# Optimization experiments

Hardware: AMD Instinct MI355X
Metric: run time of the kernel (lower is better)

Reference implementation:

```python
import jax, jax.numpy as jnp
import numpy as np

N_NODES = 50000
N_EDGES = 800000
IN_DIM = 128
HEADS1, D1 = 4, 16   # hidden_dim // 4 = 16, concat -> 64
HID = HEADS1 * D1    # 64
OUT_DIM = 40
NEG_SLOPE = 0.2      # PyG GATConv default


def setup_inputs() -> dict:
    key = jax.random.key(0)
    ks = jax.random.split(key, 11)
    x = jax.random.normal(ks[0], (N_NODES, IN_DIM), dtype=jnp.float32)
    edge_index = jax.random.randint(ks[1], (2, N_EDGES), 0, N_NODES)
    s1 = 1.0 / np.sqrt(IN_DIM)
    s2 = 1.0 / np.sqrt(HID)
    return {
        "x": x,
        "edge_index": edge_index,
        "W1": jax.random.normal(ks[2], (IN_DIM, HEADS1 * D1), dtype=jnp.float32) * s1,
        "a_src1": jax.random.normal(ks[3], (HEADS1, D1), dtype=jnp.float32) * s2,
        "a_dst1": jax.random.normal(ks[4], (HEADS1, D1), dtype=jnp.float32) * s2,
        "b1": jnp.zeros((HID,), dtype=jnp.float32),
        "W2": jax.random.normal(ks[5], (HID, OUT_DIM), dtype=jnp.float32) * s2,
        "a_src2": jax.random.normal(ks[6], (1, OUT_DIM), dtype=jnp.float32) * s2,
        "a_dst2": jax.random.normal(ks[7], (1, OUT_DIM), dtype=jnp.float32) * s2,
        "b2": jnp.zeros((OUT_DIM,), dtype=jnp.float32),
    }


def gat_conv(x, src, dst, W, a_src, a_dst, b, heads, d, n_nodes):
    # linear projection, split into heads: [N, H, d]
    h = (x @ W).reshape(n_nodes, heads, d)
    # per-node attention logits: [N, H]
    alpha_src = jnp.einsum("nhd,hd->nh", h, a_src)
    alpha_dst = jnp.einsum("nhd,hd->nh", h, a_dst)
    # edge attention coefficients
    e = jax.nn.leaky_relu(alpha_src[src] + alpha_dst[dst], NEG_SLOPE)  # [E, H]
    # segment softmax over incoming edges of each destination node
    e_max = jax.ops.segment_max(e, dst, num_segments=n_nodes)
    e_max = jnp.where(jnp.isfinite(e_max), e_max, 0.0)
    e_exp = jnp.exp(e - e_max[dst])
    denom = jax.ops.segment_sum(e_exp, dst, num_segments=n_nodes)
    alpha = e_exp / (denom[dst] + 1e-16)  # [E, H]
    # weighted scatter-aggregate of source messages
    out = jax.ops.segment_sum(h[src] * alpha[..., None], dst, num_segments=n_nodes)
    return out.reshape(n_nodes, heads * d) + b


def reference(x, edge_index, W1, a_src1, a_dst1, b1, W2, a_src2, a_dst2, b2):
    n = x.shape[0]
    # PyG GATConv add_self_loops=True
    loop = jnp.arange(n, dtype=edge_index.dtype)
    src = jnp.concatenate([edge_index[0], loop])
    dst = jnp.concatenate([edge_index[1], loop])
    h = jax.nn.relu(gat_conv(x, src, dst, W1, a_src1, a_dst1, b1, HEADS1, D1, n))
    # dropout is identity in eval mode
    h = gat_conv(h, src, dst, W2, a_src2, a_dst2, b2, 1, OUT_DIM, n)
    return jax.nn.log_softmax(h, axis=1)
```

## Files before the change

### kernel.cpp

```cpp
#include <hip/hip_runtime.h>
#include <hip/hip_fp16.h>
#include <math.h>

#define NN    50000
#define NE0   800000
#define NE    850000
#define INDIM 128
#define HID   64
#define OUTD  40

#define NB    391
#define BSH   7
#define BCAP  3072

typedef unsigned short u16;

union __align__(16) SMa {
    struct { float Wl[INDIM * HID]; float xs[64 * 132]; } g;
    struct { int lh[NB]; int lbase[NB]; unsigned ebuf[3328]; } b;
};

__global__ __launch_bounds__(256, 2) void k_binG1(
    const int* __restrict__ ei, int* __restrict__ bcur, unsigned int* __restrict__ epack,
    const float* __restrict__ x, const float* __restrict__ W1,
    const float* __restrict__ a_s, const float* __restrict__ a_d,
    __half* __restrict__ h1h, float* __restrict__ asrc1, float* __restrict__ adst1)
{
    __shared__ SMa sm;
    const int tid = threadIdx.x;

    if (blockIdx.x < 256) {
        const int CH = (NE + 255) / 256;
        const int e0 = blockIdx.x * CH;
        const int e1 = (e0 + CH < NE) ? e0 + CH : NE;
        const int cnt = e1 - e0;

        for (int i = tid; i < NB; i += 256) sm.b.lh[i] = 0;
        __syncthreads();
        for (int i = tid; i < cnt; i += 256) {
            int e = e0 + i;
            int src, dst;
            if (e < NE0) { src = ei[e]; dst = ei[NE0 + e]; }
            else         { src = e - NE0; dst = src; }
            int bkt = dst >> BSH;
            sm.b.ebuf[i] = (unsigned)src | ((unsigned)(dst & 127) << 16) | ((unsigned)bkt << 23);
            atomicAdd(&sm.b.lh[bkt], 1);
        }
        __syncthreads();
        for (int i = tid; i < NB; i += 256) {
            int c = sm.b.lh[i];
            sm.b.lbase[i] = c ? (i * BCAP + atomicAdd(&bcur[i], c)) : 0;
            sm.b.lh[i] = 0;
        }
        __syncthreads();
        for (int i = tid; i < cnt; i += 256) {
            unsigned rec = sm.b.ebuf[i];
            int bkt = rec >> 23;
            int lpos = atomicAdd(&sm.b.lh[bkt], 1);
            epack[sm.b.lbase[bkt] + lpos] = rec & 0x7FFFFFu;
        }
        return;
    }

    const int r0 = (blockIdx.x - 256) * 64;

    const float4* W4 = (const float4*)W1;
    float4* Wl4 = (float4*)sm.g.Wl;
#pragma unroll
    for (int i = 0; i < 8; ++i) Wl4[tid + i * 256] = W4[tid + i * 256];

    const float4* x4 = (const float4*)x;
#pragma unroll
    for (int i = 0; i < 8; ++i) {
        int idx = tid + i * 256;
        int row = idx >> 5;
        int k4  = idx & 31;
        int nr = r0 + row;
        float4 v = make_float4(0.f, 0.f, 0.f, 0.f);
        if (nr < NN) v = x4[(size_t)nr * 32 + k4];
        *(float4*)&sm.g.xs[row * 132 + k4 * 4] = v;
    }
    __syncthreads();

    const int rg = tid >> 4;
    const int cg = tid & 15;
    const int c4 = cg * 4;
    const float as0 = a_s[c4], as1v = a_s[c4+1], as2v = a_s[c4+2], as3v = a_s[c4+3];
    const float ad0 = a_d[c4], ad1v = a_d[c4+1], ad2v = a_d[c4+2], ad3v = a_d[c4+3];

    float acc[4][4];
#pragma unroll
    for (int i = 0; i < 4; ++i)
#pragma unroll
        for (int j = 0; j < 4; ++j) acc[i][j] = 0.f;

#pragma unroll 4
    for (int k4 = 0; k4 < 32; ++k4) {
        float4 xv[4];
#pragma unroll
        for (int i = 0; i < 4; ++i)
            xv[i] = *(const float4*)&sm.g.xs[(rg * 4 + i) * 132 + k4 * 4];
        const float* wp = &sm.g.Wl[(k4 * 4) * HID + c4];
        float4 w0 = *(const float4*)(wp);
        float4 w1 = *(const float4*)(wp + HID);
        float4 w2 = *(const float4*)(wp + 2 * HID);
        float4 w3 = *(const float4*)(wp + 3 * HID);
#pragma unroll
        for (int i = 0; i < 4; ++i) {
            acc[i][0] += xv[i].x * w0.x + xv[i].y * w1.x + xv[i].z * w2.x + xv[i].w * w3.x;
            acc[i][1] += xv[i].x * w0.y + xv[i].y * w1.y + xv[i].z * w2.y + xv[i].w * w3.y;
            acc[i][2] += xv[i].x * w0.z + xv[i].y * w1.z + xv[i].z * w2.z + xv[i].w * w3.z;
            acc[i][3] += xv[i].x * w0.w + xv[i].y * w1.w + xv[i].z * w2.w + xv[i].w * w3.w;
        }
    }

#pragma unroll
    for (int i = 0; i < 4; ++i) {
        const int n = r0 + rg * 4 + i;
        if (n < NN) {
            __half2 ha = __floats2half2_rn(acc[i][0], acc[i][1]);
            __half2 hb = __floats2half2_rn(acc[i][2], acc[i][3]);
            *(__half2*)&h1h[(size_t)n * HID + c4]     = ha;
            *(__half2*)&h1h[(size_t)n * HID + c4 + 2] = hb;
        }
        float ps = acc[i][0] * as0 + acc[i][1] * as1v + acc[i][2] * as2v + acc[i][3] * as3v;
        float pd = acc[i][0] * ad0 + acc[i][1] * ad1v + acc[i][2] * ad2v + acc[i][3] * ad3v;
        ps += __shfl_xor(ps, 1); ps += __shfl_xor(ps, 2);
        pd += __shfl_xor(pd, 1); pd += __shfl_xor(pd, 2);
        if ((cg & 3) == 0 && n < NN) {
            int head = cg >> 2;
            asrc1[n * 4 + head] = ps;
            adst1[n * 4 + head] = pd;
        }
    }
}

__global__ __launch_bounds__(256) void k_csr(
    const int* __restrict__ bcur, const unsigned int* __restrict__ epack,
    int* __restrict__ off_s, int* __restrict__ off_e, u16* __restrict__ esrc)
{
    __shared__ int lh[128];
    __shared__ int lcur[128];
    __shared__ int sblk;
    const int tid = threadIdx.x, lane = tid & 63;
    const int b = blockIdx.x;
    const int e0 = b * BCAP;
    const int cnt = bcur[b];

    if (tid < 128) lh[tid] = 0;
    __syncthreads();
    for (int i = tid; i < cnt; i += 256)
        atomicAdd(&lh[epack[e0 + i] >> 16], 1);
    __syncthreads();

    int v = 0, incl = 0;
    if (tid < 128) {
        v = lh[tid];
        incl = v;
#pragma unroll
        for (int s = 1; s < 64; s <<= 1) {
            int t = __shfl_up(incl, s);
            if (lane >= s) incl += t;
        }
    }
    if (tid == 63) sblk = incl;
    __syncthreads();
    if (tid >= 64 && tid < 128) incl += sblk;
    if (tid < 128) {
        int ex = e0 + incl - v;
        lcur[tid] = ex;
        int gd = b * 128 + tid;
        if (gd < NN) { off_s[gd] = ex; off_e[gd] = ex + v; }
    }
    __syncthreads();

    for (int i = tid; i < cnt; i += 256) {
        unsigned int p = epack[e0 + i];
        int pos = atomicAdd(&lcur[p >> 16], 1);
        esrc[pos] = (u16)(p & 0xFFFFu);
    }
}

__global__ __launch_bounds__(256) void k_fagg1g2(
    const int* __restrict__ off_s, const int* __restrict__ off_e,
    const u16* __restrict__ esrc, const float* __restrict__ asrc1,
    const float* __restrict__ adst1,
    const __half* __restrict__ h1h, const float* __restrict__ b1,
    const float* __restrict__ W2, const float* __restrict__ a_s2,
    const float* __restrict__ a_d2,
    __half* __restrict__ h2h, float* __restrict__ asrc2, float* __restrict__ adst2)
{
    __shared__ __align__(16) float W2l[HID * OUTD];
    __shared__ __align__(16) float hml[16][72];
    __shared__ float s_a2s[OUTD], s_a2d[OUTD];
    __shared__ float s_ps[16], s_pd[16];
    const int tid = threadIdx.x;

    {
        const float4* W24 = (const float4*)W2;
        float4* W2l4 = (float4*)W2l;
        for (int i = tid; i < (HID * OUTD) / 4; i += 256) W2l4[i] = W24[i];
        if (tid < OUTD) { s_a2s[tid] = a_s2[tid]; s_a2d[tid] = a_d2[tid]; }
        if (tid < 16)   { s_ps[tid] = 0.f; s_pd[tid] = 0.f; }
    }

    const int wv = tid >> 6, lane = tid & 63;
    const int g = lane >> 4, li = lane & 15;
    const int r = wv * 4 + g;
    const int n = blockIdx.x * 16 + r;
    const int s0 = off_s[n], s1 = off_e[n];
    const int hp = li >> 2;
    const float adst = adst1[n * 4 + hp];
    const int last = s1 - 1;

    float l = 0.f, a0 = 0.f, a1 = 0.f, a2 = 0.f, a3 = 0.f;
    const char* hb = (const char*)h1h;

    int sxA[8];
#pragma unroll
    for (int j = 0; j < 8; ++j) {
        int ix = s0 + j;
        sxA[j] = esrc[ix < s1 ? ix : last];
    }
    for (int t = s0; t < s1; t += 8) {
        float ax[8];
#pragma unroll
        for (int j = 0; j < 8; ++j) ax[j] = asrc1[sxA[j] * 4 + hp];
        uint2 raw[8];
#pragma unroll
        for (int j = 0; j < 8; ++j)
            raw[j] = *(const uint2*)(hb + ((size_t)sxA[j] * 128 + li * 8));
        int sxB[8];
        const int t2 = t + 8;
#pragma unroll
        for (int j = 0; j < 8; ++j) {
            int ix = t2 + j;
            sxB[j] = esrc[ix < s1 ? ix : last];
        }
#pragma unroll
        for (int j = 0; j < 8; ++j) {
            float e = ax[j] + adst;
            e = (e > 0.f) ? e : 0.2f * e;
            float w = __expf(e);
            w = ((t + j) < s1) ? w : 0.f;
            float2 f0 = __half22float2(*(__half2*)&raw[j].x);
            float2 f1 = __half22float2(*(__half2*)&raw[j].y);
            l  += w;
            a0 += w * f0.x;
            a1 += w * f0.y;
            a2 += w * f1.x;
            a3 += w * f1.y;
        }
#pragma unroll
        for (int j = 0; j < 8; ++j) sxA[j] = sxB[j];
    }

    {
        float rcp = 1.f / l;
        float4 bv = *(const float4*)&b1[li * 4];
        float o0 = fmaxf(a0 * rcp + bv.x, 0.f);
        float o1 = fmaxf(a1 * rcp + bv.y, 0.f);
        float o2 = fmaxf(a2 * rcp + bv.z, 0.f);
        float o3 = fmaxf(a3 * rcp + bv.w, 0.f);
        *(float4*)&hml[r][li * 4] = make_float4(o0, o1, o2, o3);
    }
    __syncthreads();

    if (tid < 160) {
        const int rr = tid / 10;
        const int c4 = (tid - rr * 10) * 4;
        float4 acc = make_float4(0.f, 0.f, 0.f, 0.f);
#pragma unroll 4
        for (int k4 = 0; k4 < 16; ++k4) {
            float4 hv = *(const float4*)&hml[rr][k4 * 4];
            const float* wp = &W2l[(k4 * 4) * OUTD + c4];
            float4 w0 = *(const float4*)(wp);
            float4 w1 = *(const float4*)(wp + OUTD);
            float4 w2 = *(const float4*)(wp + 2 * OUTD);
            float4 w3 = *(const float4*)(wp + 3 * OUTD);
            acc.x += hv.x * w0.x + hv.y * w1.x + hv.z * w2.x + hv.w * w3.x;
            acc.y += hv.x * w0.y + hv.y * w1.y + hv.z * w2.y + hv.w * w3.y;
            acc.z += hv.x * w0.z + hv.y * w1.z + hv.z * w2.z + hv.w * w3.z;
            acc.w += hv.x * w0.w + hv.y * w1.w + hv.z * w2.w + hv.w * w3.w;
        }
        const int n2 = blockIdx.x * 16 + rr;
        __half2 ha = __floats2half2_rn(acc.x, acc.y);
        __half2 hc = __floats2half2_rn(acc.z, acc.w);
        uint2 st;
        st.x = *(unsigned*)&ha;
        st.y = *(unsigned*)&hc;
        *(uint2*)((char*)h2h + ((size_t)n2 * 80 + c4 * 2)) = st;
        float ps = acc.x * s_a2s[c4] + acc.y * s_a2s[c4 + 1] + acc.z * s_a2s[c4 + 2] + acc.w * s_a2s[c4 + 3];
        float pd = acc.x * s_a2d[c4] + acc.y * s_a2d[c4 + 1] + acc.z * s_a2d[c4 + 2] + acc.w * s_a2d[c4 + 3];
        atomicAdd(&s_ps[rr], ps);
        atomicAdd(&s_pd[rr], pd);
    }
    __syncthreads();
    if (tid < 16) {
        const int n2 = blockIdx.x * 16 + tid;
        asrc2[n2] = s_ps[tid];
        adst2[n2] = s_pd[tid];
    }
}

__global__ __launch_bounds__(256) void k_fagg2(
    const int* __restrict__ off_s, const int* __restrict__ off_e,
    const u16* __restrict__ esrc, const float* __restrict__ asrc2,
    const float* __restrict__ adst2,
    const __half* __restrict__ h2h, const float* __restrict__ b2,
    float* __restrict__ out)
{
    __shared__ float svals[24][OUTD];
    const int wv = threadIdx.x >> 6, lane = threadIdx.x & 63;
    const int g = lane / 10;
    const int li = lane - g * 10;
    const bool ga = (g < 6);
    const int n = blockIdx.x * 24 + wv * 6 + (ga ? g : 0);
    const bool valid = ga && (n < NN);
    const int s0 = valid ? off_s[n] : 0;
    const int s1 = valid ? off_e[n] : 0;
    const float adst = valid ? adst2[n] : 0.f;
    const int last = (s1 > 0) ? s1 - 1 : 0;

    float l = 0.f, a0 = 0.f, a1 = 0.f, a2 = 0.f, a3 = 0.f;
    const char* hb = (const char*)h2h;

    int sxA[8];
#pragma unroll
    for (int j = 0; j < 8; ++j) {
        int ix = s0 + j;
        sxA[j] = esrc[ix < s1 ? ix : last];
    }
    for (int t = s0; t < s1; t += 8) {
        float ax[8];
#pragma unroll
        for (int j = 0; j < 8; ++j) ax[j] = asrc2[sxA[j]];
        uint2 raw[8];
#pragma unroll
        for (int j = 0; j < 8; ++j)
            raw[j] = *(const uint2*)(hb + ((size_t)sxA[j] * 80 + li * 8));
        int sxB[8];
        const int t2 = t + 8;
#pragma unroll
        for (int j = 0; j < 8; ++j) {
            int ix = t2 + j;
            sxB[j] = esrc[ix < s1 ? ix : last];
        }
#pragma unroll
        for (int j = 0; j < 8; ++j) {
            float e = ax[j] + adst;
            e = (e > 0.f) ? e : 0.2f * e;
            float w = __expf(e);
            w = ((t + j) < s1) ? w : 0.f;
            float2 f0 = __half22float2(*(__half2*)&raw[j].x);
            float2 f1 = __half22float2(*(__half2*)&raw[j].y);
            l  += w;
            a0 += w * f0.x;
            a1 += w * f0.y;
            a2 += w * f1.x;
            a3 += w * f1.y;
        }
#pragma unroll
        for (int j = 0; j < 8; ++j) sxA[j] = sxB[j];
    }
    if (valid) {
        float rcp = 1.f / l;
        float4 bv = *(const float4*)&b2[li * 4];
        int r = wv * 6 + g;
        svals[r][li * 4]     = a0 * rcp + bv.x;
        svals[r][li * 4 + 1] = a1 * rcp + bv.y;
        svals[r][li * 4 + 2] = a2 * rcp + bv.z;
        svals[r][li * 4 + 3] = a3 * rcp + bv.w;
    }
    __syncthreads();

    for (int r = wv; r < 24; r += 4) {
        int n2 = blockIdx.x * 24 + r;
        if (n2 >= NN) continue;
        float v = (lane < OUTD) ? svals[r][lane] : -1e30f;
        float mx = v;
#pragma unroll
        for (int o = 32; o; o >>= 1) mx = fmaxf(mx, __shfl_xor(mx, o));
        float ex = (lane < OUTD) ? __expf(v - mx) : 0.f;
        float sm = ex;
#pragma unroll
        for (int o = 32; o; o >>= 1) sm += __shfl_xor(sm, o);
        if (lane < OUTD) out[(size_t)n2 * OUTD + lane] = v - mx - __logf(sm);
    }
}

extern "C" void kernel_launch(void* const* d_in, const int* in_sizes, int n_in,
                              void* d_out, int out_size, void* d_ws, size_t ws_size,
                              hipStream_t stream)
{
    const float* x   = (const float*)d_in[0];
    const int*   ei  = (const int*)  d_in[1];
    const float* W1  = (const float*)d_in[2];
    const float* as1 = (const float*)d_in[3];
    const float* ad1 = (const float*)d_in[4];
    const float* b1  = (const float*)d_in[5];
    const float* W2  = (const float*)d_in[6];
    const float* as2 = (const float*)d_in[7];
    const float* ad2 = (const float*)d_in[8];
    const float* b2  = (const float*)d_in[9];
    float* out = (float*)d_out;

    char* ws = (char*)d_ws;
    __half* h1h   = (__half*)(ws);
    __half* h2h   = (__half*)(ws +  6400000);
    float*  asrc1 = (float*) (ws + 10400000);
    float*  adst1 = (float*) (ws + 11200000);
    float*  asrc2 = (float*) (ws + 12000000);
    float*  adst2 = (float*) (ws + 12200000);
    int*    off_s = (int*)   (ws + 12400000);
    int*    off_e = (int*)   (ws + 12600000);
    unsigned int* epack = (unsigned int*)(ws + 12800000);
    u16*    esrc  = (u16*)   (ws + 17604608);
    int*    bcur  = (int*)   (ws + 20006912);

    hipMemsetAsync(bcur, 0, NB * sizeof(int), stream);
    hipLaunchKernelGGL(k_binG1,  dim3(1038), dim3(256), 0, stream,
                       ei, bcur, epack, x, W1, as1, ad1, h1h, asrc1, adst1);
    hipLaunchKernelGGL(k_csr,    dim3(NB),   dim3(256), 0, stream,
                       bcur, epack, off_s, off_e, esrc);
    hipLaunchKernelGGL(k_fagg1g2, dim3(3125), dim3(256), 0, stream,
                       off_s, off_e, esrc, asrc1, adst1, h1h, b1, W2, as2, ad2, h2h, asrc2, adst2);
    hipLaunchKernelGGL(k_fagg2,  dim3(2084), dim3(256), 0, stream,
                       off_s, off_e, esrc, asrc2, adst2, h2h, b2, out);
}
```

Measured before the change: 182.4 us.

## Drop LDS staging in fused bin/GEMM kernel and double binning blocks

The fused binning and layer-1 projection kernel no longer stages W1 and x tiles in shared memory. The GEMM part now reads x rows and W1 directly from global memory through the cache, which shrinks the LDS footprint enough to raise launch bounds from 2 to 4 blocks per SM. The binning part is split across twice as many blocks with half-size edge buffers, giving more parallelism and smaller per-block LDS. The cost is repeated uncoalesced float4 global loads of x and W1 per thread instead of reuse from LDS.

```diff
diff --git a/kernel.cpp b/kernel.cpp
--- a/kernel.cpp
+++ b/kernel.cpp
@@ -13,29 +13,29 @@
 #define BSH   7
 #define BCAP  3072
 
+#define BINB  512
+#define G1B   782
+
 typedef unsigned short u16;
 
-union __align__(16) SMa {
-    struct { float Wl[INDIM * HID]; float xs[64 * 132]; } g;
-    struct { int lh[NB]; int lbase[NB]; unsigned ebuf[3328]; } b;
-};
-
-__global__ __launch_bounds__(256, 2) void k_binG1(
+__global__ __launch_bounds__(256, 4) void k_binG1(
     const int* __restrict__ ei, int* __restrict__ bcur, unsigned int* __restrict__ epack,
     const float* __restrict__ x, const float* __restrict__ W1,
     const float* __restrict__ a_s, const float* __restrict__ a_d,
     __half* __restrict__ h1h, float* __restrict__ asrc1, float* __restrict__ adst1)
 {
-    __shared__ SMa sm;
+    __shared__ int lh[NB];
+    __shared__ int lbase[NB];
+    __shared__ unsigned ebuf[1664];
     const int tid = threadIdx.x;
 
-    if (blockIdx.x < 256) {
-        const int CH = (NE + 255) / 256;
+    if (blockIdx.x < BINB) {
+        const int CH = (NE + BINB - 1) / BINB;
         const int e0 = blockIdx.x * CH;
         const int e1 = (e0 + CH < NE) ? e0 + CH : NE;
         const int cnt = e1 - e0;
 
-        for (int i = tid; i < NB; i += 256) sm.b.lh[i] = 0;
+        for (int i = tid; i < NB; i += 256) lh[i] = 0;
         __syncthreads();
         for (int i = tid; i < cnt; i += 256) {
             int e = e0 + i;
@@ -43,51 +43,41 @@
             if (e < NE0) { src = ei[e]; dst = ei[NE0 + e]; }
             else         { src = e - NE0; dst = src; }
             int bkt = dst >> BSH;
-            sm.b.ebuf[i] = (unsigned)src | ((unsigned)(dst & 127) << 16) | ((unsigned)bkt << 23);
-            atomicAdd(&sm.b.lh[bkt], 1);
+            ebuf[i] = (unsigned)src | ((unsigned)(dst & 127) << 16) | ((unsigned)bkt << 23);
+            atomicAdd(&lh[bkt], 1);
         }
         __syncthreads();
         for (int i = tid; i < NB; i += 256) {
-            int c = sm.b.lh[i];
-            sm.b.lbase[i] = c ? (i * BCAP + atomicAdd(&bcur[i], c)) : 0;
-            sm.b.lh[i] = 0;
+            int c = lh[i];
+            lbase[i] = c ? (i * BCAP + atomicAdd(&bcur[i], c)) : 0;
+            lh[i] = 0;
         }
         __syncthreads();
         for (int i = tid; i < cnt; i += 256) {
-            unsigned rec = sm.b.ebuf[i];
+            unsigned rec = ebuf[i];
             int bkt = rec >> 23;
-            int lpos = atomicAdd(&sm.b.lh[bkt], 1);
-            epack[sm.b.lbase[bkt] + lpos] = rec & 0x7FFFFFu;
+            int lpos = atomicAdd(&lh[bkt], 1);
+            epack[lbase[bkt] + lpos] = rec & 0x7FFFFFu;
         }
         return;
     }
 
-    const int r0 = (blockIdx.x - 256) * 64;
-
-    const float4* W4 = (const float4*)W1;
-    float4* Wl4 = (float4*)sm.g.Wl;
-#pragma unroll
-    for (int i = 0; i < 8; ++i) Wl4[tid + i * 256] = W4[tid + i * 256];
-
-    const float4* x4 = (const float4*)x;
-#pragma unroll
-    for (int i = 0; i < 8; ++i) {
-        int idx = tid + i * 256;
-        int row = idx >> 5;
-        int k4  = idx & 31;
-        int nr = r0 + row;
-        float4 v = make_float4(0.f, 0.f, 0.f, 0.f);
-        if (nr < NN) v = x4[(size_t)nr * 32 + k4];
-        *(float4*)&sm.g.xs[row * 132 + k4 * 4] = v;
-    }
-    __syncthreads();
-
+    const int r0 = (blockIdx.x - BINB) * 64;
     const int rg = tid >> 4;
     const int cg = tid & 15;
     const int c4 = cg * 4;
     const float as0 = a_s[c4], as1v = a_s[c4+1], as2v = a_s[c4+2], as3v = a_s[c4+3];
     const float ad0 = a_d[c4], ad1v = a_d[c4+1], ad2v = a_d[c4+2], ad3v = a_d[c4+3];
 
+    int row[4];
+#pragma unroll
+    for (int i = 0; i < 4; ++i) {
+        int nr = r0 + rg * 4 + i;
+        row[i] = (nr < NN) ? nr : NN - 1;
+    }
+
+    const float4* x4 = (const float4*)x;
+
     float acc[4][4];
 #pragma unroll
     for (int i = 0; i < 4; ++i)
@@ -99,8 +89,8 @@
         float4 xv[4];
 #pragma unroll
         for (int i = 0; i < 4; ++i)
-            xv[i] = *(const float4*)&sm.g.xs[(rg * 4 + i) * 132 + k4 * 4];
-        const float* wp = &sm.g.Wl[(k4 * 4) * HID + c4];
+            xv[i] = x4[(size_t)row[i] * 32 + k4];
+        const float* wp = &W1[(k4 * 4) * HID + c4];
         float4 w0 = *(const float4*)(wp);
         float4 w1 = *(const float4*)(wp + HID);
         float4 w2 = *(const float4*)(wp + 2 * HID);
@@ -419,7 +409,7 @@
     int*    bcur  = (int*)   (ws + 20006912);
 
     hipMemsetAsync(bcur, 0, NB * sizeof(int), stream);
-    hipLaunchKernelGGL(k_binG1,  dim3(1038), dim3(256), 0, stream,
+    hipLaunchKernelGGL(k_binG1,  dim3(BINB + G1B), dim3(256), 0, stream,
                        ei, bcur, epack, x, W1, as1, ad1, h1h, asrc1, adst1);
     hipLaunchKernelGGL(k_csr,    dim3(NB),   dim3(256), 0, stream,
                        bcur, epack, off_s, off_e, esrc);
```

After: 197.3 us. 1.08x slower.
